# Kernel tuning notes

Measured on AMD Instinct MI355X. Metric: run time of the kernel, lower is better.

## Reference

```python
import jax, jax.numpy as jnp
import numpy as np

D_MODEL = 1024

def setup_inputs() -> dict:
    key = jax.random.key(0)
    k1, k2, k3, k4, k5 = jax.random.split(key, 5)
    x = jax.random.normal(k1, (4, 2048, D_MODEL), dtype=jnp.float32)
    # torch nn.Linear weights: [out_features, in_features]
    W_qkv = jax.random.normal(k2, (3 * D_MODEL, D_MODEL), dtype=jnp.float32) * (1.0 / np.sqrt(D_MODEL))
    b_qkv = jax.random.normal(k3, (3 * D_MODEL,), dtype=jnp.float32) * 0.01
    W_proj = jax.random.normal(k4, (D_MODEL, D_MODEL), dtype=jnp.float32) * (1.0 / np.sqrt(D_MODEL))
    b_proj = jax.random.normal(k5, (D_MODEL,), dtype=jnp.float32) * 0.01
    return {"x": x, "W_qkv": W_qkv, "b_qkv": b_qkv, "W_proj": W_proj, "b_proj": b_proj}

def reference(x, W_qkv, b_qkv, W_proj, b_proj):
    # qkv projection: x @ W.T + b  (torch Linear convention)
    qkv = jnp.einsum('bsd,ed->bse', x, W_qkv) + b_qkv  # [B,S,3D]
    q, k, v = jnp.split(qkv, 3, axis=-1)               # each [B,S,D]
    scale = 1.0 / jnp.sqrt(jnp.asarray(q.shape[-1], dtype=q.dtype))
    scores = jnp.einsum('bqd,bkd->bqk', q, k) * scale   # [B,S,S]
    attn = jax.nn.softmax(scores, axis=-1)
    out = jnp.einsum('bqk,bkd->bqd', attn, v)           # [B,S,D]
    return jnp.einsum('bsd,ed->bse', out, W_proj) + b_proj
```

## Files before the change

### kernel.cpp

```cpp
#include <hip/hip_runtime.h>
#include <stdint.h>
#include <stddef.h>


typedef __attribute__((ext_vector_type(8))) short bf16x8;
typedef __attribute__((ext_vector_type(4))) float f32x4;

__device__ __forceinline__ unsigned short f2bf(float f) {
  unsigned u = __float_as_uint(f);
  u += 0x7fffu + ((u >> 16) & 1u);
  return (unsigned short)(u >> 16);
}
__device__ __forceinline__ float bf2f(unsigned short h) {
  return __uint_as_float(((unsigned)h) << 16);
}

typedef const __attribute__((address_space(1))) void* gas_ptr;
typedef __attribute__((address_space(3))) void* las_ptr;

__device__ __forceinline__ void gload_lds16(const void* g, void* l) {
  __builtin_amdgcn_global_load_lds((gas_ptr)(uintptr_t)g,
                                   (las_ptr)(uint32_t)(uintptr_t)l, 16, 0, 0);
}

__device__ __forceinline__ f32x4 mfma16(bf16x8 a, bf16x8 b, f32x4 c) {
  return __builtin_amdgcn_mfma_f32_16x16x32_bf16(a, b, c, 0, 0, 0);
}

__global__ __launch_bounds__(256) void cvt_f32_bf16(
    const float* __restrict__ in, unsigned short* __restrict__ out, int n) {
  int i = (blockIdx.x * blockDim.x + threadIdx.x) * 4;
  int stride = gridDim.x * blockDim.x * 4;
  for (; i < n; i += stride) {
    float4 v = *reinterpret_cast<const float4*>(in + i);
    ushort4 o;
    o.x = f2bf(v.x); o.y = f2bf(v.y); o.z = f2bf(v.z); o.w = f2bf(v.w);
    *reinterpret_cast<ushort4*>(out + i) = o;
  }
}


__device__ __forceinline__ void stage_gf(const unsigned short* __restrict__ P,
                                         int ld, unsigned short* dst, int wid,
                                         int lane) {
#pragma unroll
  for (int c = 0; c < 4; ++c) {
    int s = (c * 4 + wid) * 64 + lane;
    int row = s >> 3, g = s & 7;
    gload_lds16(P + (size_t)row * ld + ((g ^ (row & 7)) * 8),
                dst + (c * 4 + wid) * 512);
  }
}

template <bool OUT_BF16, bool HAS_BIAS, bool EXPOUT, bool RSCALE>
__global__ __launch_bounds__(256, 2) void gf(
    const unsigned short* __restrict__ A, const unsigned short* __restrict__ B,
    void* __restrict__ Cv, const float* __restrict__ bias,
    const float* __restrict__ rowsc, int rsStride,
    int K, int lda, int ldb, int ldc,
    long long strideA, long long strideB, long long strideC, float alpha) {
  __shared__ unsigned short lds[2][2][128 * 64];

  const int bz = blockIdx.z;
  const int gx = gridDim.x;
  int lin = blockIdx.y * gx + blockIdx.x;
  int bx, by;
  {
    const int nwg = gx * gridDim.y;
    const int q = nwg >> 3;
    lin = (lin & 7) * q + (lin >> 3);
    const int t = lin >> 6, r = lin & 63;
    const int tilesX = gx >> 3;
    bx = (t % tilesX) * 8 + (r & 7);
    by = (t / tilesX) * 8 + (r >> 3);
  }
  const int rowBase = by * 128;
  const int colBase = bx * 128;

  const unsigned short* Ap = A + (size_t)bz * (size_t)strideA + (size_t)rowBase * lda;
  const unsigned short* Bp = B + (size_t)bz * (size_t)strideB + (size_t)colBase * ldb;

  const int tid = threadIdx.x;
  const int wid = tid >> 6;
  const int lane = tid & 63;
  const int wr = wid >> 1;
  const int wc = wid & 1;
  const int fr = lane & 15;
  const int kgi = lane >> 4;

  const int nt = K >> 6;

  f32x4 acc[4][4] = {};

  stage_gf(Ap, lda, &lds[0][0][0], wid, lane);
  stage_gf(Bp, ldb, &lds[0][1][0], wid, lane);
  asm volatile("s_waitcnt vmcnt(0)" ::: "memory");
  __builtin_amdgcn_sched_barrier(0);
  __builtin_amdgcn_s_barrier();

  for (int t = 0; t < nt; ++t) {
    const int cur = t & 1;
    if (t + 1 < nt) {
      stage_gf(Ap + (size_t)(t + 1) * 64, lda, &lds[cur ^ 1][0][0], wid, lane);
      stage_gf(Bp + (size_t)(t + 1) * 64, ldb, &lds[cur ^ 1][1][0], wid, lane);
    }
    const unsigned short* sAc = &lds[cur][0][0];
    const unsigned short* sBc = &lds[cur][1][0];

    bf16x8 af[4][2], bv[4][2];
#pragma unroll
    for (int m = 0; m < 4; ++m) {
      int row = wr * 64 + m * 16 + fr;
      int r7 = row & 7;
      af[m][0] = *(const bf16x8*)&sAc[row * 64 + ((kgi ^ r7) * 8)];
      af[m][1] = *(const bf16x8*)&sAc[row * 64 + (((4 + kgi) ^ r7) * 8)];
    }
#pragma unroll
    for (int n = 0; n < 4; ++n) {
      int row = wc * 64 + n * 16 + fr;
      int r7 = row & 7;
      bv[n][0] = *(const bf16x8*)&sBc[row * 64 + ((kgi ^ r7) * 8)];
      bv[n][1] = *(const bf16x8*)&sBc[row * 64 + (((4 + kgi) ^ r7) * 8)];
    }
    asm volatile("s_waitcnt lgkmcnt(0)" ::: "memory");
    __builtin_amdgcn_sched_barrier(0);
    __builtin_amdgcn_s_setprio(1);
#pragma unroll
    for (int m = 0; m < 4; ++m)
#pragma unroll
      for (int n = 0; n < 4; ++n) {
        acc[m][n] = mfma16(af[m][0], bv[n][0], acc[m][n]);
        acc[m][n] = mfma16(af[m][1], bv[n][1], acc[m][n]);
      }
    __builtin_amdgcn_s_setprio(0);
    __builtin_amdgcn_sched_barrier(0);
    asm volatile("s_waitcnt vmcnt(0)" ::: "memory");
    __builtin_amdgcn_sched_barrier(0);
    __builtin_amdgcn_s_barrier();
  }

  const int rg = (lane >> 4) * 4;
  const float* rsb = RSCALE ? rowsc + (size_t)bz * (size_t)rsStride : nullptr;

  if (OUT_BF16) {
    unsigned short* cl = &lds[0][0][0];
#pragma unroll
    for (int m = 0; m < 4; ++m) {
      int rloc0 = wr * 64 + m * 16 + rg;
      float rs4[4];
      if (RSCALE) {
#pragma unroll
        for (int j = 0; j < 4; ++j) rs4[j] = rsb[rowBase + rloc0 + j];
      }
#pragma unroll
      for (int n = 0; n < 4; ++n) {
        int cloc = wc * 64 + n * 16 + fr;
        float bvs = 0.0f;
        if (HAS_BIAS) bvs = bias[colBase + cloc];
#pragma unroll
        for (int j = 0; j < 4; ++j) {
          int row = rloc0 + j;
          float v = acc[m][n][j] * alpha;
          if (EXPOUT) v = __expf(v);
          else v += bvs;
          if (RSCALE) v *= rs4[j];
          int gW = cloc >> 3;
          int gS = (gW & 8) | ((gW & 7) ^ (row & 7));
          cl[row * 128 + gS * 8 + (cloc & 7)] = f2bf(v);
        }
      }
    }
    __syncthreads();
    unsigned short* Cb =
        reinterpret_cast<unsigned short*>(Cv) + (size_t)bz * (size_t)strideC;
#pragma unroll
    for (int i = 0; i < 8; ++i) {
      int slot = i * 256 + tid;
      int row = slot >> 4, g = slot & 15;
      int gS = (g & 8) | ((g & 7) ^ (row & 7));
      bf16x8 v = *(const bf16x8*)&cl[row * 128 + gS * 8];
      *(bf16x8*)&Cb[(size_t)(rowBase + row) * ldc + colBase + g * 8] = v;
    }
  } else {
    float* clf = reinterpret_cast<float*>(&lds[0][0][0]);
#pragma unroll
    for (int m = 0; m < 4; ++m) {
      int rloc0 = wr * 64 + m * 16 + rg;
      float rs4[4];
      if (RSCALE) {
#pragma unroll
        for (int j = 0; j < 4; ++j) rs4[j] = rsb[rowBase + rloc0 + j];
      }
#pragma unroll
      for (int n = 0; n < 4; ++n) {
        int cloc = wc * 64 + n * 16 + fr;
        float bvs = 0.0f;
        if (HAS_BIAS) bvs = bias[colBase + cloc];
#pragma unroll
        for (int j = 0; j < 4; ++j) {
          int row = rloc0 + j;
          float v = acc[m][n][j] * alpha;
          if (EXPOUT) v = __expf(v);
          else v += bvs;
          if (RSCALE) v *= rs4[j];
          int gW = cloc >> 2;
          int gS = (gW & 24) | ((gW & 7) ^ (row & 7));
          clf[row * 128 + gS * 4 + (cloc & 3)] = v;
        }
      }
    }
    __syncthreads();
    float* Cf = reinterpret_cast<float*>(Cv) + (size_t)bz * (size_t)strideC;
#pragma unroll
    for (int i = 0; i < 16; ++i) {
      int slot = i * 256 + tid;
      int row = slot >> 5, g = slot & 31;
      int gS = (g & 24) | ((g & 7) ^ (row & 7));
      float4 v = *(const float4*)&clf[row * 128 + gS * 4];
      *(float4*)&Cf[(size_t)(rowBase + row) * ldc + colBase + g * 4] = v;
    }
  }
}

__global__ void transpose_v(const unsigned short* __restrict__ vbuf,
                            unsigned short* __restrict__ vt) {
  __shared__ unsigned short tile[32][33];
  const int b = blockIdx.z;
  const int d0 = blockIdx.x * 32;
  const int s0 = blockIdx.y * 32;
  const int tx = threadIdx.x, ty = threadIdx.y;
#pragma unroll
  for (int i = 0; i < 32; i += 8)
    tile[ty + i][tx] =
        vbuf[(size_t)(b * 2048 + s0 + ty + i) * 1024 + d0 + tx];
  __syncthreads();
#pragma unroll
  for (int i = 0; i < 32; i += 8)
    vt[((size_t)b * 1024 + d0 + ty + i) * 2048 + s0 + tx] = tile[tx][ty + i];
}

__global__ __launch_bounds__(256) void rowsum_inv(
    const unsigned short* __restrict__ p, float* __restrict__ inv) {
  __shared__ float red[4];
  const size_t row = blockIdx.x;
  const unsigned short* pr = p + row * 2048;
  const int tid = threadIdx.x;

  ushort4 u0 = *reinterpret_cast<const ushort4*>(pr + tid * 8);
  ushort4 u1 = *reinterpret_cast<const ushort4*>(pr + tid * 8 + 4);
  float sum = bf2f(u0.x) + bf2f(u0.y) + bf2f(u0.z) + bf2f(u0.w) +
              bf2f(u1.x) + bf2f(u1.y) + bf2f(u1.z) + bf2f(u1.w);
#pragma unroll
  for (int off = 32; off; off >>= 1) sum += __shfl_xor(sum, off);
  if ((tid & 63) == 0) red[tid >> 6] = sum;
  __syncthreads();
  if (tid == 0) inv[row] = 1.0f / (red[0] + red[1] + red[2] + red[3]);
}

extern "C" void kernel_launch(void* const* d_in, const int* in_sizes, int n_in,
                              void* d_out, int out_size, void* d_ws, size_t ws_size,
                              hipStream_t stream) {
  const float* x     = (const float*)d_in[0];
  const float* Wqkv  = (const float*)d_in[1];
  const float* bqkv  = (const float*)d_in[2];
  const float* Wproj = (const float*)d_in[3];
  const float* bproj = (const float*)d_in[4];
  float* out = (float*)d_out;

  char* ws = (char*)d_ws;
  unsigned short* qk   = (unsigned short*)(ws + 0);
  unsigned short* vbuf = (unsigned short*)(ws + 33554432);
  unsigned short* xatt = (unsigned short*)(ws + 50331648);
  unsigned short* wq   = (unsigned short*)(ws + 67108864);
  float*          invs = (float*)(ws + 67108864);
  unsigned short* wp   = (unsigned short*)(ws + 73400320);
  unsigned short* vt   = (unsigned short*)(ws + 75497472);
  unsigned short* sc   = (unsigned short*)(ws + 92274688);

  dim3 blk256(256);

  cvt_f32_bf16<<<2048, blk256, 0, stream>>>(x, xatt, 8192 * 1024);
  cvt_f32_bf16<<<1024, blk256, 0, stream>>>(Wqkv, wq, 3072 * 1024);
  cvt_f32_bf16<<<512, blk256, 0, stream>>>(Wproj, wp, 1024 * 1024);

  gf<true, true, false, false><<<dim3(16, 64, 1), blk256, 0, stream>>>(
      xatt, wq, qk, bqkv, nullptr, 0,
      1024, 1024, 1024, 2048, 0, 0, 0, 1.0f);

  gf<true, true, false, false><<<dim3(8, 64, 1), blk256, 0, stream>>>(
      xatt, wq + 2048 * 1024, vbuf, bqkv + 2048, nullptr, 0,
      1024, 1024, 1024, 1024, 0, 0, 0, 1.0f);

  transpose_v<<<dim3(32, 64, 4), dim3(32, 8), 0, stream>>>(vbuf, vt);

  gf<true, false, true, false><<<dim3(16, 16, 4), blk256, 0, stream>>>(
      qk, qk + 1024, sc, nullptr, nullptr, 0,
      1024, 2048, 2048, 2048,
      2048LL * 2048, 2048LL * 2048, 2048LL * 2048, 0.03125f);

  rowsum_inv<<<8192, blk256, 0, stream>>>(sc, invs);

  gf<true, false, false, true><<<dim3(8, 16, 4), blk256, 0, stream>>>(
      sc, vt, xatt, nullptr, invs, 2048,
      2048, 2048, 2048, 1024,
      2048LL * 2048, 1024LL * 2048, 2048LL * 1024, 1.0f);

  gf<false, true, false, false><<<dim3(8, 64, 1), blk256, 0, stream>>>(
      xatt, wp, out, bproj, nullptr, 0,
      1024, 1024, 1024, 1024, 0, 0, 0, 1.0f);
}
```

Baseline: 189.2 us.

## Halve GEMM K-tile to 32 and raise occupancy to four blocks per CU

```diff
diff --git a/kernel.cpp b/kernel.cpp
--- a/kernel.cpp
+++ b/kernel.cpp
@@ -40,26 +40,26 @@
 }
 
 
-__device__ __forceinline__ void stage_gf(const unsigned short* __restrict__ P,
-                                         int ld, unsigned short* dst, int wid,
-                                         int lane) {
-#pragma unroll
-  for (int c = 0; c < 4; ++c) {
-    int s = (c * 4 + wid) * 64 + lane;
-    int row = s >> 3, g = s & 7;
-    gload_lds16(P + (size_t)row * ld + ((g ^ (row & 7)) * 8),
-                dst + (c * 4 + wid) * 512);
+__device__ __forceinline__ void stage32(const unsigned short* __restrict__ P,
+                                        int ld, unsigned short* dst, int tid) {
+  const int w = tid >> 6, l = tid & 63;
+  const int rr = l >> 2;
+  const int cswz = (((l & 3) ^ ((l >> 3) & 3)) * 8);
+#pragma unroll
+  for (int c = 0; c < 2; ++c) {
+    int r = c * 64 + w * 16 + rr;
+    gload_lds16(P + (size_t)r * ld + cswz, dst + c * 2048 + w * 512);
   }
 }
 
 template <bool OUT_BF16, bool HAS_BIAS, bool EXPOUT, bool RSCALE>
-__global__ __launch_bounds__(256, 2) void gf(
+__global__ __launch_bounds__(256, 4) void gp(
     const unsigned short* __restrict__ A, const unsigned short* __restrict__ B,
     void* __restrict__ Cv, const float* __restrict__ bias,
     const float* __restrict__ rowsc, int rsStride,
     int K, int lda, int ldb, int ldc,
     long long strideA, long long strideB, long long strideC, float alpha) {
-  __shared__ unsigned short lds[2][2][128 * 64];
+  __shared__ unsigned short lds[2][2][128 * 32];
 
   const int bz = blockIdx.z;
   const int gx = gridDim.x;
@@ -87,56 +87,37 @@
   const int wc = wid & 1;
   const int fr = lane & 15;
   const int kgi = lane >> 4;
-
-  const int nt = K >> 6;
+  const int rcol = ((kgi ^ ((fr >> 1) & 3)) * 8);
+
+  const int nt = K >> 5;
 
   f32x4 acc[4][4] = {};
 
-  stage_gf(Ap, lda, &lds[0][0][0], wid, lane);
-  stage_gf(Bp, ldb, &lds[0][1][0], wid, lane);
-  asm volatile("s_waitcnt vmcnt(0)" ::: "memory");
-  __builtin_amdgcn_sched_barrier(0);
-  __builtin_amdgcn_s_barrier();
+  stage32(Ap, lda, &lds[0][0][0], tid);
+  stage32(Bp, ldb, &lds[0][1][0], tid);
+  __syncthreads();
 
   for (int t = 0; t < nt; ++t) {
     const int cur = t & 1;
     if (t + 1 < nt) {
-      stage_gf(Ap + (size_t)(t + 1) * 64, lda, &lds[cur ^ 1][0][0], wid, lane);
-      stage_gf(Bp + (size_t)(t + 1) * 64, ldb, &lds[cur ^ 1][1][0], wid, lane);
+      stage32(Ap + (size_t)(t + 1) * 32, lda, &lds[cur ^ 1][0][0], tid);
+      stage32(Bp + (size_t)(t + 1) * 32, ldb, &lds[cur ^ 1][1][0], tid);
     }
     const unsigned short* sAc = &lds[cur][0][0];
     const unsigned short* sBc = &lds[cur][1][0];
-
-    bf16x8 af[4][2], bv[4][2];
-#pragma unroll
-    for (int m = 0; m < 4; ++m) {
-      int row = wr * 64 + m * 16 + fr;
-      int r7 = row & 7;
-      af[m][0] = *(const bf16x8*)&sAc[row * 64 + ((kgi ^ r7) * 8)];
-      af[m][1] = *(const bf16x8*)&sAc[row * 64 + (((4 + kgi) ^ r7) * 8)];
-    }
-#pragma unroll
-    for (int n = 0; n < 4; ++n) {
-      int row = wc * 64 + n * 16 + fr;
-      int r7 = row & 7;
-      bv[n][0] = *(const bf16x8*)&sBc[row * 64 + ((kgi ^ r7) * 8)];
-      bv[n][1] = *(const bf16x8*)&sBc[row * 64 + (((4 + kgi) ^ r7) * 8)];
-    }
-    asm volatile("s_waitcnt lgkmcnt(0)" ::: "memory");
-    __builtin_amdgcn_sched_barrier(0);
-    __builtin_amdgcn_s_setprio(1);
+    bf16x8 af[4], bv[4];
 #pragma unroll
     for (int m = 0; m < 4; ++m)
-#pragma unroll
-      for (int n = 0; n < 4; ++n) {
-        acc[m][n] = mfma16(af[m][0], bv[n][0], acc[m][n]);
-        acc[m][n] = mfma16(af[m][1], bv[n][1], acc[m][n]);
-      }
-    __builtin_amdgcn_s_setprio(0);
-    __builtin_amdgcn_sched_barrier(0);
-    asm volatile("s_waitcnt vmcnt(0)" ::: "memory");
-    __builtin_amdgcn_sched_barrier(0);
-    __builtin_amdgcn_s_barrier();
+      af[m] = *(const bf16x8*)&sAc[(wr * 64 + m * 16 + fr) * 32 + rcol];
+#pragma unroll
+    for (int n = 0; n < 4; ++n)
+      bv[n] = *(const bf16x8*)&sBc[(wc * 64 + n * 16 + fr) * 32 + rcol];
+#pragma unroll
+    for (int m = 0; m < 4; ++m)
+#pragma unroll
+      for (int n = 0; n < 4; ++n)
+        acc[m][n] = mfma16(af[m], bv[n], acc[m][n]);
+    __syncthreads();
   }
 
   const int rg = (lane >> 4) * 4;
@@ -183,41 +164,44 @@
     }
   } else {
     float* clf = reinterpret_cast<float*>(&lds[0][0][0]);
-#pragma unroll
-    for (int m = 0; m < 4; ++m) {
-      int rloc0 = wr * 64 + m * 16 + rg;
-      float rs4[4];
-      if (RSCALE) {
-#pragma unroll
-        for (int j = 0; j < 4; ++j) rs4[j] = rsb[rowBase + rloc0 + j];
-      }
-#pragma unroll
-      for (int n = 0; n < 4; ++n) {
-        int cloc = wc * 64 + n * 16 + fr;
-        float bvs = 0.0f;
-        if (HAS_BIAS) bvs = bias[colBase + cloc];
-#pragma unroll
-        for (int j = 0; j < 4; ++j) {
-          int row = rloc0 + j;
-          float v = acc[m][n][j] * alpha;
-          if (EXPOUT) v = __expf(v);
-          else v += bvs;
-          if (RSCALE) v *= rs4[j];
-          int gW = cloc >> 2;
-          int gS = (gW & 24) | ((gW & 7) ^ (row & 7));
-          clf[row * 128 + gS * 4 + (cloc & 3)] = v;
+    float* Cf = reinterpret_cast<float*>(Cv) + (size_t)bz * (size_t)strideC;
+#pragma unroll
+    for (int half = 0; half < 2; ++half) {
+      if (wr == half) {
+#pragma unroll
+        for (int m = 0; m < 4; ++m) {
+          int rloc0 = m * 16 + rg;
+          float rs4[4];
+          if (RSCALE) {
+#pragma unroll
+            for (int j = 0; j < 4; ++j)
+              rs4[j] = rsb[rowBase + half * 64 + rloc0 + j];
+          }
+#pragma unroll
+          for (int n = 0; n < 4; ++n) {
+            int cloc = wc * 64 + n * 16 + fr;
+            float bvs = 0.0f;
+            if (HAS_BIAS) bvs = bias[colBase + cloc];
+#pragma unroll
+            for (int j = 0; j < 4; ++j) {
+              float v = acc[m][n][j] * alpha;
+              if (EXPOUT) v = __expf(v);
+              else v += bvs;
+              if (RSCALE) v *= rs4[j];
+              clf[(rloc0 + j) * 128 + cloc] = v;
+            }
+          }
         }
       }
-    }
-    __syncthreads();
-    float* Cf = reinterpret_cast<float*>(Cv) + (size_t)bz * (size_t)strideC;
-#pragma unroll
-    for (int i = 0; i < 16; ++i) {
-      int slot = i * 256 + tid;
-      int row = slot >> 5, g = slot & 31;
-      int gS = (g & 24) | ((g & 7) ^ (row & 7));
-      float4 v = *(const float4*)&clf[row * 128 + gS * 4];
-      *(float4*)&Cf[(size_t)(rowBase + row) * ldc + colBase + g * 4] = v;
+      __syncthreads();
+#pragma unroll
+      for (int i = 0; i < 8; ++i) {
+        int slot = i * 256 + tid;
+        int row = slot >> 5, g = slot & 31;
+        float4 v = *(const float4*)&clf[row * 128 + g * 4];
+        *(float4*)&Cf[(size_t)(rowBase + half * 64 + row) * ldc + colBase + g * 4] = v;
+      }
+      __syncthreads();
     }
   }
 }
@@ -283,29 +267,29 @@
   cvt_f32_bf16<<<1024, blk256, 0, stream>>>(Wqkv, wq, 3072 * 1024);
   cvt_f32_bf16<<<512, blk256, 0, stream>>>(Wproj, wp, 1024 * 1024);
 
-  gf<true, true, false, false><<<dim3(16, 64, 1), blk256, 0, stream>>>(
+  gp<true, true, false, false><<<dim3(16, 64, 1), blk256, 0, stream>>>(
       xatt, wq, qk, bqkv, nullptr, 0,
       1024, 1024, 1024, 2048, 0, 0, 0, 1.0f);
 
-  gf<true, true, false, false><<<dim3(8, 64, 1), blk256, 0, stream>>>(
+  gp<true, true, false, false><<<dim3(8, 64, 1), blk256, 0, stream>>>(
       xatt, wq + 2048 * 1024, vbuf, bqkv + 2048, nullptr, 0,
       1024, 1024, 1024, 1024, 0, 0, 0, 1.0f);
 
   transpose_v<<<dim3(32, 64, 4), dim3(32, 8), 0, stream>>>(vbuf, vt);
 
-  gf<true, false, true, false><<<dim3(16, 16, 4), blk256, 0, stream>>>(
+  gp<true, false, true, false><<<dim3(16, 16, 4), blk256, 0, stream>>>(
       qk, qk + 1024, sc, nullptr, nullptr, 0,
       1024, 2048, 2048, 2048,
       2048LL * 2048, 2048LL * 2048, 2048LL * 2048, 0.03125f);
 
   rowsum_inv<<<8192, blk256, 0, stream>>>(sc, invs);
 
-  gf<true, false, false, true><<<dim3(8, 16, 4), blk256, 0, stream>>>(
+  gp<true, false, false, true><<<dim3(8, 16, 4), blk256, 0, stream>>>(
       sc, vt, xatt, nullptr, invs, 2048,
       2048, 2048, 2048, 1024,
       2048LL * 2048, 1024LL * 2048, 2048LL * 1024, 1.0f);
 
-  gf<false, true, false, false><<<dim3(8, 64, 1), blk256, 0, stream>>>(
+  gp<false, true, false, false><<<dim3(8, 64, 1), blk256, 0, stream>>>(
       xatt, wp, out, bproj, nullptr, 0,
       1024, 1024, 1024, 1024, 0, 0, 0, 1.0f);
 }
```

New measurement: 217.2 us. 14.8% more time.

## Fuse V transpose into projection epilogue and rowsum into score GEMM

Applied to the files above, without the earlier changes.

```diff
diff --git a/kernel.cpp b/kernel.cpp
--- a/kernel.cpp
+++ b/kernel.cpp
@@ -39,7 +39,6 @@
   }
 }
 
-
 __device__ __forceinline__ void stage_gf(const unsigned short* __restrict__ P,
                                          int ld, unsigned short* dst, int wid,
                                          int lane) {
@@ -52,11 +51,12 @@
   }
 }
 
-template <bool OUT_BF16, bool HAS_BIAS, bool EXPOUT, bool RSCALE>
+template <bool OUT_BF16, bool HAS_BIAS, bool EXPOUT, bool RSCALE,
+          bool TRANSOUT, bool RSUM>
 __global__ __launch_bounds__(256, 2) void gf(
     const unsigned short* __restrict__ A, const unsigned short* __restrict__ B,
     void* __restrict__ Cv, const float* __restrict__ bias,
-    const float* __restrict__ rowsc, int rsStride,
+    const float* __restrict__ rowsc, float* __restrict__ rsum, int rsStride,
     int K, int lda, int ldb, int ldc,
     long long strideA, long long strideB, long long strideC, float alpha) {
   __shared__ unsigned short lds[2][2][128 * 64];
@@ -142,7 +142,34 @@
   const int rg = (lane >> 4) * 4;
   const float* rsb = RSCALE ? rowsc + (size_t)bz * (size_t)rsStride : nullptr;
 
-  if (OUT_BF16) {
+  if (TRANSOUT) {
+    unsigned short* cl = &lds[0][0][0];
+#pragma unroll
+    for (int m = 0; m < 4; ++m) {
+      int rloc0 = wr * 64 + m * 16 + rg;
+#pragma unroll
+      for (int n = 0; n < 4; ++n) {
+        int cloc = wc * 64 + n * 16 + fr;
+        float bvs = HAS_BIAS ? bias[colBase + cloc] : 0.0f;
+#pragma unroll
+        for (int j = 0; j < 4; ++j) {
+          float v = acc[m][n][j] * alpha + bvs;
+          cl[cloc * 136 + rloc0 + j] = f2bf(v);
+        }
+      }
+    }
+    __syncthreads();
+    const int b = rowBase >> 11;
+    const int s0 = rowBase & 2047;
+    unsigned short* Vt = reinterpret_cast<unsigned short*>(Cv);
+#pragma unroll
+    for (int i = 0; i < 8; ++i) {
+      int slot = i * 256 + tid;
+      int d = slot >> 4, sg = slot & 15;
+      bf16x8 v = *(const bf16x8*)&cl[d * 136 + sg * 8];
+      *(bf16x8*)&Vt[((size_t)(b * 1024 + colBase + d)) * 2048 + s0 + sg * 8] = v;
+    }
+  } else if (OUT_BF16) {
     unsigned short* cl = &lds[0][0][0];
 #pragma unroll
     for (int m = 0; m < 4; ++m) {
@@ -180,6 +207,17 @@
       int gS = (g & 8) | ((g & 7) ^ (row & 7));
       bf16x8 v = *(const bf16x8*)&cl[row * 128 + gS * 8];
       *(bf16x8*)&Cb[(size_t)(rowBase + row) * ldc + colBase + g * 8] = v;
+      if (RSUM) {
+        float s8 = 0.0f;
+#pragma unroll
+        for (int k = 0; k < 8; ++k) s8 += bf2f((unsigned short)v[k]);
+        s8 += __shfl_xor(s8, 1);
+        s8 += __shfl_xor(s8, 2);
+        s8 += __shfl_xor(s8, 4);
+        s8 += __shfl_xor(s8, 8);
+        if ((lane & 15) == 0)
+          rsum[((size_t)bz * 2048 + rowBase + row) * 16 + bx] = s8;
+      }
     }
   } else {
     float* clf = reinterpret_cast<float*>(&lds[0][0][0]);
@@ -222,39 +260,14 @@
   }
 }
 
-__global__ void transpose_v(const unsigned short* __restrict__ vbuf,
-                            unsigned short* __restrict__ vt) {
-  __shared__ unsigned short tile[32][33];
-  const int b = blockIdx.z;
-  const int d0 = blockIdx.x * 32;
-  const int s0 = blockIdx.y * 32;
-  const int tx = threadIdx.x, ty = threadIdx.y;
-#pragma unroll
-  for (int i = 0; i < 32; i += 8)
-    tile[ty + i][tx] =
-        vbuf[(size_t)(b * 2048 + s0 + ty + i) * 1024 + d0 + tx];
-  __syncthreads();
-#pragma unroll
-  for (int i = 0; i < 32; i += 8)
-    vt[((size_t)b * 1024 + d0 + ty + i) * 2048 + s0 + tx] = tile[tx][ty + i];
-}
-
-__global__ __launch_bounds__(256) void rowsum_inv(
-    const unsigned short* __restrict__ p, float* __restrict__ inv) {
-  __shared__ float red[4];
-  const size_t row = blockIdx.x;
-  const unsigned short* pr = p + row * 2048;
-  const int tid = threadIdx.x;
-
-  ushort4 u0 = *reinterpret_cast<const ushort4*>(pr + tid * 8);
-  ushort4 u1 = *reinterpret_cast<const ushort4*>(pr + tid * 8 + 4);
-  float sum = bf2f(u0.x) + bf2f(u0.y) + bf2f(u0.z) + bf2f(u0.w) +
-              bf2f(u1.x) + bf2f(u1.y) + bf2f(u1.z) + bf2f(u1.w);
-#pragma unroll
-  for (int off = 32; off; off >>= 1) sum += __shfl_xor(sum, off);
-  if ((tid & 63) == 0) red[tid >> 6] = sum;
-  __syncthreads();
-  if (tid == 0) inv[row] = 1.0f / (red[0] + red[1] + red[2] + red[3]);
+__global__ __launch_bounds__(256) void inv_from_partial(
+    const float* __restrict__ rs, float* __restrict__ inv) {
+  int r = blockIdx.x * 256 + threadIdx.x;
+  const float4* p = reinterpret_cast<const float4*>(rs + (size_t)r * 16);
+  float4 a = p[0], b = p[1], c = p[2], d = p[3];
+  float s = a.x + a.y + a.z + a.w + b.x + b.y + b.z + b.w +
+            c.x + c.y + c.z + c.w + d.x + d.y + d.z + d.w;
+  inv[r] = 1.0f / s;
 }
 
 extern "C" void kernel_launch(void* const* d_in, const int* in_sizes, int n_in,
@@ -269,10 +282,10 @@
 
   char* ws = (char*)d_ws;
   unsigned short* qk   = (unsigned short*)(ws + 0);
-  unsigned short* vbuf = (unsigned short*)(ws + 33554432);
   unsigned short* xatt = (unsigned short*)(ws + 50331648);
   unsigned short* wq   = (unsigned short*)(ws + 67108864);
-  float*          invs = (float*)(ws + 67108864);
+  float*          invs = (float*)(ws + 33554432);
+  float*          rsp  = (float*)(ws + 33554432 + 65536);
   unsigned short* wp   = (unsigned short*)(ws + 73400320);
   unsigned short* vt   = (unsigned short*)(ws + 75497472);
   unsigned short* sc   = (unsigned short*)(ws + 92274688);
@@ -283,29 +296,27 @@
   cvt_f32_bf16<<<1024, blk256, 0, stream>>>(Wqkv, wq, 3072 * 1024);
   cvt_f32_bf16<<<512, blk256, 0, stream>>>(Wproj, wp, 1024 * 1024);
 
-  gf<true, true, false, false><<<dim3(16, 64, 1), blk256, 0, stream>>>(
-      xatt, wq, qk, bqkv, nullptr, 0,
+  gf<true, true, false, false, false, false><<<dim3(16, 64, 1), blk256, 0, stream>>>(
+      xatt, wq, qk, bqkv, nullptr, nullptr, 0,
       1024, 1024, 1024, 2048, 0, 0, 0, 1.0f);
 
-  gf<true, true, false, false><<<dim3(8, 64, 1), blk256, 0, stream>>>(
-      xatt, wq + 2048 * 1024, vbuf, bqkv + 2048, nullptr, 0,
-      1024, 1024, 1024, 1024, 0, 0, 0, 1.0f);
-
-  transpose_v<<<dim3(32, 64, 4), dim3(32, 8), 0, stream>>>(vbuf, vt);
-
-  gf<true, false, true, false><<<dim3(16, 16, 4), blk256, 0, stream>>>(
-      qk, qk + 1024, sc, nullptr, nullptr, 0,
+  gf<true, true, false, false, true, false><<<dim3(8, 64, 1), blk256, 0, stream>>>(
+      xatt, wq + 2048 * 1024, vt, bqkv + 2048, nullptr, nullptr, 0,
+      1024, 1024, 1024, 2048, 0, 0, 0, 1.0f);
+
+  gf<true, false, true, false, false, true><<<dim3(16, 16, 4), blk256, 0, stream>>>(
+      qk, qk + 1024, sc, nullptr, nullptr, rsp, 0,
       1024, 2048, 2048, 2048,
       2048LL * 2048, 2048LL * 2048, 2048LL * 2048, 0.03125f);
 
-  rowsum_inv<<<8192, blk256, 0, stream>>>(sc, invs);
-
-  gf<true, false, false, true><<<dim3(8, 16, 4), blk256, 0, stream>>>(
-      sc, vt, xatt, nullptr, invs, 2048,
+  inv_from_partial<<<32, blk256, 0, stream>>>(rsp, invs);
+
+  gf<true, false, false, true, false, false><<<dim3(8, 16, 4), blk256, 0, stream>>>(
+      sc, vt, xatt, nullptr, invs, nullptr, 2048,
       2048, 2048, 2048, 1024,
       2048LL * 2048, 1024LL * 2048, 2048LL * 1024, 1.0f);
 
-  gf<false, true, false, false><<<dim3(8, 64, 1), blk256, 0, stream>>>(
-      xatt, wp, out, bproj, nullptr, 0,
+  gf<false, true, false, false, false, false><<<dim3(8, 64, 1), blk256, 0, stream>>>(
+      xatt, wp, out, bproj, nullptr, nullptr, 0,
       1024, 1024, 1024, 1024, 0, 0, 0, 1.0f);
 }
```

Measured after the change: 176.9 us. -6.5%, faster.
